# Optimization experiments

Hardware: AMD Instinct MI355X
Metric: run time of the kernel (lower is better)

## Reference

```python
import jax, jax.numpy as jnp
import numpy as np


def _orthogonal_matrix(vectors):
    # Q = I @ H1 @ H2 @ ... ; each H = I - 2 v v^T applied as a rank-1 update:
    # Q @ H = Q - 2 (Q v) v^T  (same math as explicit matmul, O(d^2) per reflection)
    dim = vectors.shape[1]
    eye = jnp.eye(dim, dtype=vectors.dtype)

    def step(Q, v):
        vn = v / (jnp.linalg.norm(v) + 1e-8)
        Q = Q - 2.0 * jnp.outer(Q @ vn, vn)
        return Q, None

    Q, _ = jax.lax.scan(step, eye, vectors)
    return Q


def setup_inputs() -> dict:
    key = jax.random.key(0)
    k1, k2 = jax.random.split(key)
    dim, n_reflections, batch = 2048, 30, 16384
    x = jax.random.normal(k1, (batch, dim), dtype=jnp.float32)
    vectors = jax.random.normal(k2, (n_reflections, dim), dtype=jnp.float32)
    bias = jnp.zeros((dim,), dtype=jnp.float32)
    return {"x": x, "vectors": vectors, "bias": bias}


def reference(x, vectors, bias):
    Q = _orthogonal_matrix(vectors)      # [dim, dim]
    return x @ Q + bias                  # [batch, dim]
```

## Files before the change

### kernel.cpp

```cpp
#include <hip/hip_runtime.h>
#include <math.h>

#define DIM   2048
#define NREF  30
#define KPAD  32
#define BATCH 16384

typedef __attribute__((ext_vector_type(8))) short short8;
typedef __attribute__((ext_vector_type(4))) float f32x4;

#define WS_VN   0
#define WS_G    61440
#define WS_T    62464
#define WS_W2   63488
#define WS_FP1  129024
#define WS_FP2  161792
#define WS_S    194560

__device__ __forceinline__ unsigned short f2bf(float f) {
    unsigned u = __float_as_uint(f);
    u += 0x7FFF + ((u >> 16) & 1);
    return (unsigned short)(u >> 16);
}

__device__ __forceinline__ float block_reduce_sum(float s) {
    #pragma unroll
    for (int off = 32; off > 0; off >>= 1) s += __shfl_down(s, off);
    __shared__ float ws4[4];
    int t = threadIdx.x;
    if ((t & 63) == 0) ws4[t >> 6] = s;
    __syncthreads();
    return ws4[0] + ws4[1] + ws4[2] + ws4[3];
}

__global__ void k_normalize(const float* __restrict__ vec, float* __restrict__ vn) {
    int i = blockIdx.x, t = threadIdx.x;
    const float* v = vec + i * DIM;
    float s = 0.f;
    for (int d = t; d < DIM; d += 256) { float xv = v[d]; s += xv * xv; }
    float tot = block_reduce_sum(s);
    float scale = 1.f / (sqrtf(tot) + 1e-8f);
    float* o = vn + i * DIM;
    for (int d = t; d < DIM; d += 256) o[d] = v[d] * scale;
}

__global__ void k_gram(const float* __restrict__ vn, float* __restrict__ G) {
    int j = blockIdx.x, i = blockIdx.y, t = threadIdx.x;
    const float* a = vn + i * DIM;
    const float* b = vn + j * DIM;
    float s = 0.f;
    for (int d = t; d < DIM; d += 256) s += a[d] * b[d];
    float tot = block_reduce_sum(s);
    if (t == 0) G[i * NREF + j] = tot;
}

__global__ void k_T(const float* __restrict__ G, float* __restrict__ T) {
    int t = threadIdx.x;
    __shared__ float Ts[NREF][NREF];
    for (int idx = t; idx < NREF * NREF; idx += 64) Ts[idx / NREF][idx % NREF] = 0.f;
    __syncthreads();
    if (t == 0) Ts[0][0] = 2.f;
    __syncthreads();
    for (int j = 1; j < NREF; j++) {
        float val = 0.f;
        if (t < j) {
            for (int m = t; m < j; m++) val += Ts[t][m] * G[m * NREF + j];
            val *= -2.f;
        }
        if (t < j) Ts[t][j] = val;
        if (t == j) Ts[j][j] = 2.f;
        __syncthreads();
    }
    for (int idx = t; idx < NREF * NREF; idx += 64) T[idx] = Ts[idx / NREF][idx % NREF];
}

__global__ void k_w2(const float* __restrict__ vn, const float* __restrict__ T,
                     float* __restrict__ W2) {
    int d = blockIdx.x * 256 + threadIdx.x;
    float vr[NREF];
    #pragma unroll
    for (int j = 0; j < NREF; j++) vr[j] = vn[j * DIM + d];
    #pragma unroll
    for (int k = 0; k < KPAD; k++) {
        float acc = 0.f;
        if (k < NREF)
            for (int j = 0; j <= k; j++) acc += vr[j] * T[j * NREF + k];
        W2[(size_t)d * KPAD + k] = acc;
    }
}

__global__ void k_pack1(const float* __restrict__ W2, unsigned short* __restrict__ fp1) {
    int g = blockIdx.x * 256 + threadIdx.x;
    int ks = g >> 7, nt = (g >> 6) & 1, lane = g & 63;
    int q = lane >> 4, n = lane & 15;
    unsigned short tmp[8];
    #pragma unroll
    for (int j = 0; j < 8; j++)
        tmp[j] = f2bf(W2[(size_t)(ks * 32 + q * 8 + j) * KPAD + nt * 16 + n]);
    short8* out = (short8*)fp1;
    short8 v;
    #pragma unroll
    for (int j = 0; j < 8; j++) v[j] = (short)tmp[j];
    out[(ks * 2 + nt) * 64 + lane] = v;
}

__global__ void k_pack2(const float* __restrict__ vn, unsigned short* __restrict__ fp2) {
    int g = blockIdx.x * 256 + threadIdx.x;
    int ct = g >> 6, lane = g & 63;
    int q = lane >> 4, n = lane & 15;
    short8 v;
    #pragma unroll
    for (int j = 0; j < 8; j++) {
        int k = q * 8 + j;
        float f = (k < NREF) ? vn[(size_t)k * DIM + ct * 16 + n] : 0.f;
        v[j] = (short)f2bf(f);
    }
    ((short8*)fp2)[ct * 64 + lane] = v;
}

__global__ __launch_bounds__(256) void k_phase1(const float* __restrict__ x,
                                                const short8* __restrict__ fp1,
                                                unsigned short* __restrict__ S) {
    int tid = threadIdx.x;
    int wave = tid >> 6, lane = tid & 63;
    int m = lane & 15, q = lane >> 4;
    int r0 = blockIdx.x * 16;
    int kb = wave * 512;

    const float* xp = x + (size_t)(r0 + m) * DIM + kb + q * 8;

    f32x4 acc0 = {0.f, 0.f, 0.f, 0.f};
    f32x4 acc1 = {0.f, 0.f, 0.f, 0.f};

    #pragma unroll 4
    for (int ks = 0; ks < 16; ks++) {
        const float4* p = (const float4*)(xp + ks * 32);
        float4 xa = p[0];
        float4 xb = p[1];
        short8 a;
        a[0] = (short)f2bf(xa.x); a[1] = (short)f2bf(xa.y);
        a[2] = (short)f2bf(xa.z); a[3] = (short)f2bf(xa.w);
        a[4] = (short)f2bf(xb.x); a[5] = (short)f2bf(xb.y);
        a[6] = (short)f2bf(xb.z); a[7] = (short)f2bf(xb.w);
        int ksg = wave * 16 + ks;
        short8 b0 = fp1[(ksg * 2 + 0) * 64 + lane];
        short8 b1 = fp1[(ksg * 2 + 1) * 64 + lane];
        acc0 = __builtin_amdgcn_mfma_f32_16x16x32_bf16(a, b0, acc0, 0, 0, 0);
        acc1 = __builtin_amdgcn_mfma_f32_16x16x32_bf16(a, b1, acc1, 0, 0, 0);
    }

    __shared__ f32x4 red[4][64][2];
    red[wave][lane][0] = acc0;
    red[wave][lane][1] = acc1;
    __syncthreads();
    if (tid < 64) {
        f32x4 s0 = red[0][tid][0], s1 = red[0][tid][1];
        #pragma unroll
        for (int w = 1; w < 4; w++) { s0 += red[w][tid][0]; s1 += red[w][tid][1]; }
        int mq = tid & 15, qq = tid >> 4;
        #pragma unroll
        for (int reg = 0; reg < 4; reg++) {
            size_t row = r0 + qq * 4 + reg;
            S[row * KPAD + mq]      = f2bf(s0[reg]);
            S[row * KPAD + 16 + mq] = f2bf(s1[reg]);
        }
    }
}

__global__ __launch_bounds__(256) void k_phase2(const float* __restrict__ x,
                                                const unsigned short* __restrict__ S,
                                                const short8* __restrict__ fp2,
                                                const float* __restrict__ bias,
                                                float* __restrict__ y) {
    int tid = threadIdx.x;
    int wave = tid >> 6, lane = tid & 63;
    int m = lane & 15, q = lane >> 4;
    int r0 = blockIdx.x * 16;
    int c0 = wave * 512;

    short8 a = *(const short8*)(S + (size_t)(r0 + m) * KPAD + q * 8);
    f32x4 zero = {0.f, 0.f, 0.f, 0.f};
    int rbase = r0 + q * 4;

    #pragma unroll 2
    for (int t = 0; t < 32; t++) {
        int col = c0 + t * 16;
        short8 b = fp2[(wave * 32 + t) * 64 + lane];
        f32x4 p = __builtin_amdgcn_mfma_f32_16x16x32_bf16(a, b, zero, 0, 0, 0);
        int cc = col + m;
        float bi = bias[cc];
        const float* xc = x + (size_t)rbase * DIM + cc;
        float* yc = y + (size_t)rbase * DIM + cc;
        yc[0 * DIM] = xc[0 * DIM] + bi - p[0];
        yc[1 * DIM] = xc[1 * DIM] + bi - p[1];
        yc[2 * DIM] = xc[2 * DIM] + bi - p[2];
        yc[3 * DIM] = xc[3 * DIM] + bi - p[3];
    }
}

extern "C" void kernel_launch(void* const* d_in, const int* in_sizes, int n_in,
                              void* d_out, int out_size, void* d_ws, size_t ws_size,
                              hipStream_t stream) {
    const float* x    = (const float*)d_in[0];
    const float* vec  = (const float*)d_in[1];
    const float* bias = (const float*)d_in[2];
    float* out = (float*)d_out;
    float* ws  = (float*)d_ws;

    float* vn = ws + WS_VN;
    float* G  = ws + WS_G;
    float* T  = ws + WS_T;
    float* W2 = ws + WS_W2;
    unsigned short* fp1 = (unsigned short*)(ws + WS_FP1);
    unsigned short* fp2 = (unsigned short*)(ws + WS_FP2);
    unsigned short* S   = (unsigned short*)(ws + WS_S);

    k_normalize<<<NREF, 256, 0, stream>>>(vec, vn);
    k_gram<<<dim3(NREF, NREF), 256, 0, stream>>>(vn, G);
    k_T<<<1, 64, 0, stream>>>(G, T);
    k_w2<<<DIM / 256, 256, 0, stream>>>(vn, T, W2);
    k_pack1<<<32, 256, 0, stream>>>(W2, fp1);
    k_pack2<<<32, 256, 0, stream>>>(vn, fp2);
    k_phase1<<<BATCH / 16, 256, 0, stream>>>(x, (const short8*)fp1, S);
    k_phase2<<<BATCH / 16, 256, 0, stream>>>(x, S, (const short8*)fp2, bias, out);
}
```

Measured before the change: 322.1 us.

## Fuse both GEMM phases into one kernel keeping x in registers, merge prep kernels

```diff
diff --git a/kernel.cpp b/kernel.cpp
--- a/kernel.cpp
+++ b/kernel.cpp
@@ -12,10 +12,8 @@
 #define WS_VN   0
 #define WS_G    61440
 #define WS_T    62464
-#define WS_W2   63488
-#define WS_FP1  129024
-#define WS_FP2  161792
-#define WS_S    194560
+#define WS_FP1  63488
+#define WS_FP2  96256
 
 __device__ __forceinline__ unsigned short f2bf(float f) {
     unsigned u = __float_as_uint(f);
@@ -23,104 +21,119 @@
     return (unsigned short)(u >> 16);
 }
 
-__device__ __forceinline__ float block_reduce_sum(float s) {
-    #pragma unroll
-    for (int off = 32; off > 0; off >>= 1) s += __shfl_down(s, off);
-    __shared__ float ws4[4];
+__global__ void k_prep(const float* __restrict__ vec, float* __restrict__ vn,
+                       float* __restrict__ G) {
+    int b = blockIdx.x, t = threadIdx.x;
+    __shared__ float wsum[3][4];
+    if (b < NREF) {
+        const float* v = vec + b * DIM;
+        float s = 0.f;
+        for (int d = t; d < DIM; d += 256) { float xv = v[d]; s += xv * xv; }
+        #pragma unroll
+        for (int off = 32; off > 0; off >>= 1) s += __shfl_down(s, off);
+        if ((t & 63) == 0) wsum[0][t >> 6] = s;
+        __syncthreads();
+        float tot = wsum[0][0] + wsum[0][1] + wsum[0][2] + wsum[0][3];
+        float scale = 1.f / (sqrtf(tot) + 1e-8f);
+        float* o = vn + b * DIM;
+        for (int d = t; d < DIM; d += 256) o[d] = v[d] * scale;
+    } else {
+        int idx = b - NREF;
+        int i = idx / NREF, j = idx % NREF;
+        const float* a = vec + i * DIM;
+        const float* c = vec + j * DIM;
+        float sab = 0.f, saa = 0.f, sbb = 0.f;
+        for (int d = t; d < DIM; d += 256) {
+            float av = a[d], cv = c[d];
+            sab += av * cv; saa += av * av; sbb += cv * cv;
+        }
+        #pragma unroll
+        for (int off = 32; off > 0; off >>= 1) {
+            sab += __shfl_down(sab, off);
+            saa += __shfl_down(saa, off);
+            sbb += __shfl_down(sbb, off);
+        }
+        if ((t & 63) == 0) { wsum[0][t >> 6] = sab; wsum[1][t >> 6] = saa; wsum[2][t >> 6] = sbb; }
+        __syncthreads();
+        if (t == 0) {
+            float tab = wsum[0][0] + wsum[0][1] + wsum[0][2] + wsum[0][3];
+            float taa = wsum[1][0] + wsum[1][1] + wsum[1][2] + wsum[1][3];
+            float tbb = wsum[2][0] + wsum[2][1] + wsum[2][2] + wsum[2][3];
+            G[i * NREF + j] = tab / ((sqrtf(taa) + 1e-8f) * (sqrtf(tbb) + 1e-8f));
+        }
+    }
+}
+
+__global__ void k_T2(const float* __restrict__ G, float* __restrict__ T) {
     int t = threadIdx.x;
-    if ((t & 63) == 0) ws4[t >> 6] = s;
-    __syncthreads();
-    return ws4[0] + ws4[1] + ws4[2] + ws4[3];
-}
-
-__global__ void k_normalize(const float* __restrict__ vec, float* __restrict__ vn) {
-    int i = blockIdx.x, t = threadIdx.x;
-    const float* v = vec + i * DIM;
-    float s = 0.f;
-    for (int d = t; d < DIM; d += 256) { float xv = v[d]; s += xv * xv; }
-    float tot = block_reduce_sum(s);
-    float scale = 1.f / (sqrtf(tot) + 1e-8f);
-    float* o = vn + i * DIM;
-    for (int d = t; d < DIM; d += 256) o[d] = v[d] * scale;
-}
-
-__global__ void k_gram(const float* __restrict__ vn, float* __restrict__ G) {
-    int j = blockIdx.x, i = blockIdx.y, t = threadIdx.x;
-    const float* a = vn + i * DIM;
-    const float* b = vn + j * DIM;
-    float s = 0.f;
-    for (int d = t; d < DIM; d += 256) s += a[d] * b[d];
-    float tot = block_reduce_sum(s);
-    if (t == 0) G[i * NREF + j] = tot;
-}
-
-__global__ void k_T(const float* __restrict__ G, float* __restrict__ T) {
-    int t = threadIdx.x;
+    __shared__ float Gs[NREF * NREF];
     __shared__ float Ts[NREF][NREF];
-    for (int idx = t; idx < NREF * NREF; idx += 64) Ts[idx / NREF][idx % NREF] = 0.f;
-    __syncthreads();
-    if (t == 0) Ts[0][0] = 2.f;
-    __syncthreads();
-    for (int j = 1; j < NREF; j++) {
-        float val = 0.f;
-        if (t < j) {
-            for (int m = t; m < j; m++) val += Ts[t][m] * G[m * NREF + j];
-            val *= -2.f;
-        }
-        if (t < j) Ts[t][j] = val;
-        if (t == j) Ts[j][j] = 2.f;
+    for (int idx = t; idx < NREF * NREF; idx += 64) {
+        Gs[idx] = G[idx];
+        Ts[idx / NREF][idx % NREF] = 0.f;
+    }
+    __syncthreads();
+    if (t < NREF) {
+        Ts[t][t] = 2.f;
+        for (int j = t + 1; j < NREF; j++) {
+            float val = 0.f;
+            for (int mm = t; mm < j; mm++) val += Ts[t][mm] * Gs[mm * NREF + j];
+            Ts[t][j] = -2.f * val;
+        }
+    }
+    __syncthreads();
+    for (int idx = t; idx < NREF * NREF; idx += 64) T[idx] = Ts[idx / NREF][idx % NREF];
+}
+
+__global__ void k_mid(const float* __restrict__ vn, const float* __restrict__ T,
+                      unsigned short* __restrict__ fp1, unsigned short* __restrict__ fp2) {
+    int b = blockIdx.x, t = threadIdx.x;
+    if (b < 8) {
+        __shared__ float W2s[256][33];
+        int d = b * 256 + t;
+        float vr[NREF];
+        #pragma unroll
+        for (int j = 0; j < NREF; j++) vr[j] = vn[j * DIM + d];
+        #pragma unroll
+        for (int k = 0; k < KPAD; k++) {
+            float acc = 0.f;
+            if (k < NREF)
+                for (int j = 0; j <= k; j++) acc += vr[j] * T[j * NREF + k];
+            W2s[t][k] = acc;
+        }
         __syncthreads();
-    }
-    for (int idx = t; idx < NREF * NREF; idx += 64) T[idx] = Ts[idx / NREF][idx % NREF];
-}
-
-__global__ void k_w2(const float* __restrict__ vn, const float* __restrict__ T,
-                     float* __restrict__ W2) {
-    int d = blockIdx.x * 256 + threadIdx.x;
-    float vr[NREF];
-    #pragma unroll
-    for (int j = 0; j < NREF; j++) vr[j] = vn[j * DIM + d];
-    #pragma unroll
-    for (int k = 0; k < KPAD; k++) {
-        float acc = 0.f;
-        if (k < NREF)
-            for (int j = 0; j <= k; j++) acc += vr[j] * T[j * NREF + k];
-        W2[(size_t)d * KPAD + k] = acc;
-    }
-}
-
-__global__ void k_pack1(const float* __restrict__ W2, unsigned short* __restrict__ fp1) {
-    int g = blockIdx.x * 256 + threadIdx.x;
-    int ks = g >> 7, nt = (g >> 6) & 1, lane = g & 63;
-    int q = lane >> 4, n = lane & 15;
-    unsigned short tmp[8];
-    #pragma unroll
-    for (int j = 0; j < 8; j++)
-        tmp[j] = f2bf(W2[(size_t)(ks * 32 + q * 8 + j) * KPAD + nt * 16 + n]);
-    short8* out = (short8*)fp1;
-    short8 v;
-    #pragma unroll
-    for (int j = 0; j < 8; j++) v[j] = (short)tmp[j];
-    out[(ks * 2 + nt) * 64 + lane] = v;
-}
-
-__global__ void k_pack2(const float* __restrict__ vn, unsigned short* __restrict__ fp2) {
-    int g = blockIdx.x * 256 + threadIdx.x;
-    int ct = g >> 6, lane = g & 63;
-    int q = lane >> 4, n = lane & 15;
-    short8 v;
-    #pragma unroll
-    for (int j = 0; j < 8; j++) {
-        int k = q * 8 + j;
-        float f = (k < NREF) ? vn[(size_t)k * DIM + ct * 16 + n] : 0.f;
-        v[j] = (short)f2bf(f);
-    }
-    ((short8*)fp2)[ct * 64 + lane] = v;
-}
-
-__global__ __launch_bounds__(256) void k_phase1(const float* __restrict__ x,
-                                                const short8* __restrict__ fp1,
-                                                unsigned short* __restrict__ S) {
+        short8* out = (short8*)fp1;
+        #pragma unroll
+        for (int u = 0; u < 4; u++) {
+            int lf = t * 4 + u;
+            int ks_l = lf >> 7, nt = (lf >> 6) & 1, lane = lf & 63;
+            int q = lane >> 4, n = lane & 15;
+            short8 v;
+            #pragma unroll
+            for (int j = 0; j < 8; j++)
+                v[j] = (short)f2bf(W2s[ks_l * 32 + q * 8 + j][nt * 16 + n]);
+            out[((b * 8 + ks_l) * 2 + nt) * 64 + lane] = v;
+        }
+    } else {
+        int g = (b - 8) * 256 + t;
+        int ct = g >> 6, lane = g & 63;
+        int q = lane >> 4, n = lane & 15;
+        short8 v;
+        #pragma unroll
+        for (int j = 0; j < 8; j++) {
+            int k = q * 8 + j;
+            float f = (k < NREF) ? vn[(size_t)k * DIM + ct * 16 + n] : 0.f;
+            v[j] = (short)f2bf(f);
+        }
+        ((short8*)fp2)[ct * 64 + lane] = v;
+    }
+}
+
+__global__ __launch_bounds__(256, 2) void k_fused(const float* __restrict__ x,
+                                                  const short8* __restrict__ fp1,
+                                                  const short8* __restrict__ fp2,
+                                                  const float* __restrict__ bias,
+                                                  float* __restrict__ y) {
     int tid = threadIdx.x;
     int wave = tid >> 6, lane = tid & 63;
     int m = lane & 15, q = lane >> 4;
@@ -129,19 +142,23 @@
 
     const float* xp = x + (size_t)(r0 + m) * DIM + kb + q * 8;
 
+    f32x4 xr[32];
+    #pragma unroll
+    for (int ks = 0; ks < 16; ks++) {
+        xr[2 * ks]     = *(const f32x4*)(xp + ks * 32);
+        xr[2 * ks + 1] = *(const f32x4*)(xp + ks * 32 + 4);
+    }
+
     f32x4 acc0 = {0.f, 0.f, 0.f, 0.f};
     f32x4 acc1 = {0.f, 0.f, 0.f, 0.f};
-
-    #pragma unroll 4
+    #pragma unroll
     for (int ks = 0; ks < 16; ks++) {
-        const float4* p = (const float4*)(xp + ks * 32);
-        float4 xa = p[0];
-        float4 xb = p[1];
+        f32x4 xa = xr[2 * ks], xb = xr[2 * ks + 1];
         short8 a;
-        a[0] = (short)f2bf(xa.x); a[1] = (short)f2bf(xa.y);
-        a[2] = (short)f2bf(xa.z); a[3] = (short)f2bf(xa.w);
-        a[4] = (short)f2bf(xb.x); a[5] = (short)f2bf(xb.y);
-        a[6] = (short)f2bf(xb.z); a[7] = (short)f2bf(xb.w);
+        a[0] = (short)f2bf(xa[0]); a[1] = (short)f2bf(xa[1]);
+        a[2] = (short)f2bf(xa[2]); a[3] = (short)f2bf(xa[3]);
+        a[4] = (short)f2bf(xb[0]); a[5] = (short)f2bf(xb[1]);
+        a[6] = (short)f2bf(xb[2]); a[7] = (short)f2bf(xb[3]);
         int ksg = wave * 16 + ks;
         short8 b0 = fp1[(ksg * 2 + 0) * 64 + lane];
         short8 b1 = fp1[(ksg * 2 + 1) * 64 + lane];
@@ -150,6 +167,7 @@
     }
 
     __shared__ f32x4 red[4][64][2];
+    __shared__ unsigned short Slds[16][32];
     red[wave][lane][0] = acc0;
     red[wave][lane][1] = acc1;
     __syncthreads();
@@ -160,41 +178,39 @@
         int mq = tid & 15, qq = tid >> 4;
         #pragma unroll
         for (int reg = 0; reg < 4; reg++) {
-            size_t row = r0 + qq * 4 + reg;
-            S[row * KPAD + mq]      = f2bf(s0[reg]);
-            S[row * KPAD + 16 + mq] = f2bf(s1[reg]);
-        }
-    }
-}
-
-__global__ __launch_bounds__(256) void k_phase2(const float* __restrict__ x,
-                                                const unsigned short* __restrict__ S,
-                                                const short8* __restrict__ fp2,
-                                                const float* __restrict__ bias,
-                                                float* __restrict__ y) {
-    int tid = threadIdx.x;
-    int wave = tid >> 6, lane = tid & 63;
-    int m = lane & 15, q = lane >> 4;
-    int r0 = blockIdx.x * 16;
-    int c0 = wave * 512;
-
-    short8 a = *(const short8*)(S + (size_t)(r0 + m) * KPAD + q * 8);
+            Slds[qq * 4 + reg][mq]      = f2bf(s0[reg]);
+            Slds[qq * 4 + reg][16 + mq] = f2bf(s1[reg]);
+        }
+    }
+    __syncthreads();
+
+    short8 aS = *(const short8*)&Slds[m][q * 8];
     f32x4 zero = {0.f, 0.f, 0.f, 0.f};
-    int rbase = r0 + q * 4;
-
-    #pragma unroll 2
-    for (int t = 0; t < 32; t++) {
-        int col = c0 + t * 16;
-        short8 b = fp2[(wave * 32 + t) * 64 + lane];
-        f32x4 p = __builtin_amdgcn_mfma_f32_16x16x32_bf16(a, b, zero, 0, 0, 0);
-        int cc = col + m;
-        float bi = bias[cc];
-        const float* xc = x + (size_t)rbase * DIM + cc;
-        float* yc = y + (size_t)rbase * DIM + cc;
-        yc[0 * DIM] = xc[0 * DIM] + bi - p[0];
-        yc[1 * DIM] = xc[1 * DIM] + bi - p[1];
-        yc[2 * DIM] = xc[2 * DIM] + bi - p[2];
-        yc[3 * DIM] = xc[3 * DIM] + bi - p[3];
+    __shared__ float Pb[4][2][16][36];
+    const float* bp = bias + kb + q * 8;
+    float* yp0 = y + (size_t)(r0 + m) * DIM + kb + q * 8;
+
+    #pragma unroll
+    for (int u = 0; u < 16; u++) {
+        int pb = u & 1;
+        short8 b0 = fp2[(wave * 32 + 2 * u) * 64 + lane];
+        short8 b1 = fp2[(wave * 32 + 2 * u + 1) * 64 + lane];
+        f32x4 p0 = __builtin_amdgcn_mfma_f32_16x16x32_bf16(aS, b0, zero, 0, 0, 0);
+        f32x4 p1 = __builtin_amdgcn_mfma_f32_16x16x32_bf16(aS, b1, zero, 0, 0, 0);
+        #pragma unroll
+        for (int reg = 0; reg < 4; reg++) {
+            Pb[wave][pb][q * 4 + reg][m]      = p0[reg];
+            Pb[wave][pb][q * 4 + reg][16 + m] = p1[reg];
+        }
+        asm volatile("s_waitcnt lgkmcnt(0)" ::: "memory");
+        f32x4 pr0 = *(const f32x4*)&Pb[wave][pb][m][q * 8];
+        f32x4 pr1 = *(const f32x4*)&Pb[wave][pb][m][q * 8 + 4];
+        f32x4 bb0 = *(const f32x4*)(bp + u * 32);
+        f32x4 bb1 = *(const f32x4*)(bp + u * 32 + 4);
+        f32x4 o0 = xr[2 * u] + bb0 - pr0;
+        f32x4 o1 = xr[2 * u + 1] + bb1 - pr1;
+        *(f32x4*)(yp0 + u * 32)     = o0;
+        *(f32x4*)(yp0 + u * 32 + 4) = o1;
     }
 }
 
@@ -210,17 +226,11 @@
     float* vn = ws + WS_VN;
     float* G  = ws + WS_G;
     float* T  = ws + WS_T;
-    float* W2 = ws + WS_W2;
     unsigned short* fp1 = (unsigned short*)(ws + WS_FP1);
     unsigned short* fp2 = (unsigned short*)(ws + WS_FP2);
-    unsigned short* S   = (unsigned short*)(ws + WS_S);
-
-    k_normalize<<<NREF, 256, 0, stream>>>(vec, vn);
-    k_gram<<<dim3(NREF, NREF), 256, 0, stream>>>(vn, G);
-    k_T<<<1, 64, 0, stream>>>(G, T);
-    k_w2<<<DIM / 256, 256, 0, stream>>>(vn, T, W2);
-    k_pack1<<<32, 256, 0, stream>>>(W2, fp1);
-    k_pack2<<<32, 256, 0, stream>>>(vn, fp2);
-    k_phase1<<<BATCH / 16, 256, 0, stream>>>(x, (const short8*)fp1, S);
-    k_phase2<<<BATCH / 16, 256, 0, stream>>>(x, S, (const short8*)fp2, bias, out);
-}
+
+    k_prep<<<NREF + NREF * NREF, 256, 0, stream>>>(vec, vn, G);
+    k_T2<<<1, 64, 0, stream>>>(G, T);
+    k_mid<<<40, 256, 0, stream>>>(vn, T, fp1, fp2);
+    k_fused<<<BATCH / 16, 256, 0, stream>>>(x, (const short8*)fp1, (const short8*)fp2, bias, out);
+}
```

Result: faster. 277.5 us (-13.9%).
